# Performance work log

Measured on AMD Instinct MI355X. Metric: run time of the kernel, lower is better.

The kernel has to match this reference:

```python
import jax, jax.numpy as jnp
import numpy as np
import math

H, M, N = 64, 128, 128  # volume dims (m == n required by original index math)
K_NEIGH = 9
W_WIN = 3


def build_neighbor_ids(h, n, w):
    # Periodic (wrap-around) neighbor indices, matching extract_neighbour_indices
    # with m == n. Loop order: z-major, then y, then x, offsets -1..1 for w=3.
    half = w // 2
    offs = list(range(-half, half + 1))
    zi = jnp.arange(h)[:, None, None]
    yi = jnp.arange(n)[None, :, None]
    xi = jnp.arange(n)[None, None, :]
    cols = []
    for oz in offs:
        for oy in offs:
            for ox in offs:
                idx = ((zi + oz) % h) * (n * n) + ((yi + oy) % n) * n + ((xi + ox) % n)
                cols.append(idx.reshape(-1))
    return jnp.stack(cols, axis=1).astype(jnp.int32)  # [P, w^3]


def setup_inputs() -> dict:
    key = jax.random.key(0)
    k1, _ = jax.random.split(key)
    inp = jax.random.normal(k1, (H, M, N), dtype=jnp.float32)
    ksigma = jnp.ones((1, 1, 1, 1), dtype=jnp.float32)  # nn.Parameter init to sigma_m=1.0
    return {"input": inp, "ksigma": ksigma, "k": K_NEIGH, "w": W_WIN}


def reference(input, ksigma, k, w):
    h, m, n = input.shape
    ID = build_neighbor_ids(h, n, w)               # [P, nN]
    anat = input.reshape(-1)                       # [P]
    # get_knn: absolute intensity differences to each neighbor
    dist = jnp.abs(anat[ID] - anat[:, None])       # [P, nN]
    order = jnp.argsort(dist, axis=-1, stable=True)
    sID = jnp.take_along_axis(ID, order, axis=1)   # sorted neighbor indices
    IDk = sID[:, :k]                               # [P, k] top-k nearest by intensity
    Wk = anat[IDk]                                 # [P, k] neighbor intensities (feature rows)
    # get_features: per-row std (torch.std is unbiased, ddof=1)
    sigma = jnp.std(Wk, axis=1, ddof=1)            # [P]
    sigma_safe = jnp.where(sigma == 0, 1.0, sigma)
    neigh = Wk[IDk]                                # [P, k, k] gather feature rows of knn
    diff = Wk[:, None, :] - neigh + 1e-6           # pairwise_distance eps added to diff
    norm = jnp.sqrt(jnp.sum(diff * diff, axis=-1)) # [P, k] L2 pairwise distance
    ks = ksigma.reshape(())
    logits = -jnp.square(norm / sigma_safe[:, None] / (math.sqrt(2.0) * ks))
    logits = jnp.where(sigma[:, None] == 0, 0.0, logits)  # zero row -> uniform softmax
    Kw = jax.nn.softmax(logits, axis=1)            # [P, k] normalized kernel weights
    return Kw
```

## Files before the change

kernel.cpp:

```cpp
#include <hip/hip_runtime.h>
#include <hip/hip_fp16.h>
#include <array>

constexpr int HZ   = 64;
constexpr int NN   = 128;
constexpr int P    = HZ * NN * NN;
constexpr int KSEL = 9;
constexpr int NCOL = 27;
constexpr int STD  = 8;

typedef _Float16 f16x2 __attribute__((ext_vector_type(2)));

constexpr int TY = 10;
constexpr int TX = 34;

constexpr int compute_nce(int n) {
  int t = 0; while ((1 << t) < n) ++t;
  int cnt = 0;
  for (int p = 1 << (t - 1); p > 0; p >>= 1) {
    int q = 1 << (t - 1), r = 0, d = p;
    while (true) {
      for (int i = 0; i < n - d; ++i)
        if ((i & p) == r) ++cnt;
      if (q == p) break;
      d = q - p; r = p; q >>= 1;
    }
  }
  return cnt;
}
constexpr int NCE_FULL = compute_nce(NCOL);

struct CEPair { unsigned char a, b; };
constexpr std::array<CEPair, NCE_FULL> make_net() {
  std::array<CEPair, NCE_FULL> net{};
  int t = 0; while ((1 << t) < NCOL) ++t;
  int k = 0;
  for (int p = 1 << (t - 1); p > 0; p >>= 1) {
    int q = 1 << (t - 1), r = 0, d = p;
    while (true) {
      for (int i = 0; i < NCOL - d; ++i)
        if ((i & p) == r) {
          net[k].a = (unsigned char)i;
          net[k].b = (unsigned char)(i + d);
          ++k;
        }
      if (q == p) break;
      d = q - p; r = p; q >>= 1;
    }
  }
  return net;
}
constexpr auto FULLNET = make_net();

constexpr int count_pruned() {
  bool needed[NCOL] = {};
  for (int i = 0; i < KSEL; ++i) needed[i] = true;
  int cnt = 0;
  for (int e = NCE_FULL - 1; e >= 0; --e) {
    const int a = FULLNET[e].a, b = FULLNET[e].b;
    if (needed[a] || needed[b]) { needed[a] = true; needed[b] = true; ++cnt; }
  }
  return cnt;
}
constexpr int NCE = count_pruned();

constexpr std::array<CEPair, NCE> make_pruned() {
  bool needed[NCOL] = {};
  for (int i = 0; i < KSEL; ++i) needed[i] = true;
  std::array<bool, NCE_FULL> keep{};
  for (int e = NCE_FULL - 1; e >= 0; --e) {
    const int a = FULLNET[e].a, b = FULLNET[e].b;
    if (needed[a] || needed[b]) { keep[e] = true; needed[a] = true; needed[b] = true; }
  }
  std::array<CEPair, NCE> out{};
  int k = 0;
  for (int e = 0; e < NCE_FULL; ++e) if (keep[e]) out[k++] = FULLNET[e];
  return out;
}
constexpr auto NET = make_pruned();

__global__ __launch_bounds__(256) void topk8(
    const float* __restrict__ anat,
    unsigned* __restrict__ rows) {
  __shared__ float in_t[3 * TY * TX];
  __shared__ unsigned lrow[256 * STD];
  const int tid = threadIdx.x;

  const int blk = blockIdx.x;
  const int swz = ((blk & 7) << 9) | (blk >> 3);
  const int z    = swz >> 6;
  const int rest = swz & 63;
  const int y0   = ((rest >> 2) & 15) << 3;
  const int x0   = (rest & 3) << 5;
  const int xl   = tid & 31;
  const int yl   = tid >> 5;

  #pragma unroll
  for (int s = 0; s < 4; ++s) {
    const unsigned q = (unsigned)(s * 256 + tid);
    if (q < (unsigned)(3 * TY * TX)) {
      const unsigned p = q / TX;
      const unsigned r = q - p * TX;
      const unsigned pz = p / TY;
      const int zi = (int)pz, yi = (int)(p - TY * pz);
      const int zz = (z + zi - 1) & (HZ - 1);
      const int yy = (y0 + yi - 1) & (NN - 1);
      const int xg = (x0 - 1 + (int)r) & (NN - 1);
      in_t[q] = anat[(zz << 14) | (yy << 7) | xg];
    }
  }
  __syncthreads();

  const int base = (yl * TX) + xl;
  const float center = in_t[base + 1 * (TY * TX) + 1 * TX + 1];

  unsigned long long key[NCOL];
  #pragma unroll
  for (int c = 0; c < NCOL; ++c) {
    const int czi = c / 9, cyi = (c / 3) % 3, cxi = c % 3;
    const float v = in_t[base + czi * (TY * TX) + cyi * TX + cxi];
    const unsigned vb = __float_as_uint(v);
    const unsigned db = __float_as_uint(v - center) & 0x7fffffffu;
    const unsigned lo32 = ((unsigned)c << 27) | (vb >> 5);
    key[c] = ((unsigned long long)db << 32) | lo32;
  }

  #pragma unroll
  for (int e = 0; e < NCE; ++e) {
    const int a = NET[e].a, b = NET[e].b;
    const double ka = __builtin_bit_cast(double, key[a]);
    const double kb = __builtin_bit_cast(double, key[b]);
    key[a] = __builtin_bit_cast(unsigned long long, fmin(ka, kb));
    key[b] = __builtin_bit_cast(unsigned long long, fmax(ka, kb));
  }

  unsigned d[5] = {0, 0, 0, 0, 0};
  unsigned lo = 0, hi = 0;
  #pragma unroll
  for (int s = 0; s < KSEL; ++s) {
    const unsigned kl = (unsigned)key[s];
    const unsigned c  = (kl >> 27) & 31u;
    const unsigned vb = (kl & 0x07ffffffu) << 5;
    const ushort hb = __half_as_ushort(__float2half(__uint_as_float(vb)));
    d[s >> 1] |= (unsigned)hb << ((s & 1) * 16);
    if (s < 6) lo |= c << (5 * s);
    else       hi |= c << (5 * (s - 6));
  }

  unsigned* myrow = &lrow[tid * STD];
  ((uint4*)myrow)[0] = make_uint4(d[0], d[1], d[2], d[3]);
  ((uint4*)myrow)[1] = make_uint4(d[4], lo, hi, 0u);

  __syncthreads();

  uint4* rows4 = (uint4*)rows;
  const uint4* l4 = (const uint4*)lrow;
  #pragma unroll
  for (int s = 0; s < 2; ++s) {
    const unsigned q   = (unsigned)(s * 256 + tid);
    const unsigned run = q >> 6;
    const unsigned off = q & 63u;
    const unsigned vb  = (unsigned)((z << 14) | ((y0 + (int)run) << 7) | x0);
    rows4[(size_t)vb * 2 + off] = l4[run * 64 + off];
  }
}

constexpr int TROWS = 3 * TY * TX;

__global__ __launch_bounds__(256) void weights8(
    const unsigned* __restrict__ rows,
    const float* __restrict__ ksig,
    float* __restrict__ out) {
  __shared__ unsigned tile[TROWS * STD];
  const int tid = threadIdx.x;

  const int blk = blockIdx.x;
  const int swz = ((blk & 7) << 9) | (blk >> 3);
  const int z    = swz >> 6;
  const int rest = swz & 63;
  const int y0   = ((rest >> 2) & 15) << 3;
  const int x0   = (rest & 3) << 5;
  const int xl   = tid & 31;
  const int yl   = tid >> 5;

  const uint4* rows4 = (const uint4*)rows;
  uint4* t4 = (uint4*)tile;
  #pragma unroll
  for (int s = 0; s < 8; ++s) {
    const unsigned q = (unsigned)(s * 256 + tid);
    if (q < 2040u) {
      const unsigned p   = q / 68u;
      const unsigned rem = q - p * 68u;
      const unsigned r   = rem >> 1;
      const unsigned c   = rem & 1u;
      const unsigned pz  = p / 10u;
      const int zi = (int)pz, yi = (int)(p - 10u * pz);
      const int zz = (z + zi - 1) & (HZ - 1);
      const int yy = (y0 + yi - 1) & (NN - 1);
      const int xg = (x0 - 1 + (int)r) & (NN - 1);
      t4[q] = rows4[(size_t)((zz << 14) | (yy << 7) | xg) * 2 + c];
    }
  }
  __syncthreads();

  const int rho_own = (TY + (yl + 1)) * TX + (xl + 1);
  const uint4 u0 = t4[rho_own * 2], u1 = t4[rho_own * 2 + 1];
  f16x2 wh[5];
  wh[0] = __builtin_bit_cast(f16x2, u0.x);
  wh[1] = __builtin_bit_cast(f16x2, u0.y);
  wh[2] = __builtin_bit_cast(f16x2, u0.z);
  wh[3] = __builtin_bit_cast(f16x2, u0.w);
  wh[4] = __builtin_bit_cast(f16x2, u1.x);
  const unsigned lo = u1.y;
  const unsigned hi = u1.z;

  int rho[KSEL];
  #pragma unroll
  for (int j = 0; j < KSEL; ++j) {
    const unsigned c = (j < 6) ? ((lo >> (5 * j)) & 31u)
                               : ((hi >> (5 * (j - 6))) & 31u);
    const unsigned czi = (c * 57u) >> 9;
    const unsigned rem = c - 9u * czi;
    const unsigned cyi = (rem * 11u) >> 5;
    const unsigned cxi = rem - 3u * cyi;
    rho[j] = (int)czi * (TY * TX) + (yl + (int)cyi) * TX + (xl + (int)cxi);
  }
  uint4 nbuf[KSEL][2];
  #pragma unroll
  for (int j = 0; j < KSEL; ++j) {
    nbuf[j][0] = t4[rho[j] * 2];
    nbuf[j][1] = t4[rho[j] * 2 + 1];
  }

  float ws[KSEL];
  #pragma unroll
  for (int l = 0; l < KSEL; ++l) ws[l] = (float)wh[l >> 1][l & 1];
  float mean = 0.f;
  #pragma unroll
  for (int l = 0; l < KSEL; ++l) mean += ws[l];
  mean *= (1.0f / 9.0f);
  float var = 0.f;
  #pragma unroll
  for (int l = 0; l < KSEL; ++l) { const float t = ws[l] - mean; var += t * t; }
  var *= (1.0f / 8.0f);
  const float sigma = sqrtf(var);

  const float ks = ksig[0];
  const float inv = (sigma == 0.f) ? 0.f : 1.0f / (2.0f * ks * ks * sigma * sigma);

  const _Float16 epsh = (_Float16)1e-6f;
  const f16x2 eps2 = {epsh, epsh};

  float logit[KSEL];
  #pragma unroll
  for (int j = 0; j < KSEL; ++j) {
    const f16x2 nh0 = __builtin_bit_cast(f16x2, nbuf[j][0].x);
    const f16x2 nh1 = __builtin_bit_cast(f16x2, nbuf[j][0].y);
    const f16x2 nh2 = __builtin_bit_cast(f16x2, nbuf[j][0].z);
    const f16x2 nh3 = __builtin_bit_cast(f16x2, nbuf[j][0].w);
    const f16x2 nh4 = __builtin_bit_cast(f16x2, nbuf[j][1].x);
    float s = 0.f;
    f16x2 dd;
    dd = (wh[0] - nh0) + eps2; s = __builtin_amdgcn_fdot2(dd, dd, s, false);
    dd = (wh[1] - nh1) + eps2; s = __builtin_amdgcn_fdot2(dd, dd, s, false);
    dd = (wh[2] - nh2) + eps2; s = __builtin_amdgcn_fdot2(dd, dd, s, false);
    dd = (wh[3] - nh3) + eps2; s = __builtin_amdgcn_fdot2(dd, dd, s, false);
    dd = (wh[4] - nh4) + eps2; s = __builtin_amdgcn_fdot2(dd, dd, s, false);
    logit[j] = -s * inv;
  }

  float mx = logit[0];
  #pragma unroll
  for (int j = 1; j < KSEL; ++j) mx = fmaxf(mx, logit[j]);
  float sum = 0.f;
  float e[KSEL];
  #pragma unroll
  for (int j = 0; j < KSEL; ++j) { e[j] = __expf(logit[j] - mx); sum += e[j]; }
  const float rs = 1.0f / sum;

  __syncthreads();
  float* tf = (float*)tile;
  #pragma unroll
  for (int j = 0; j < KSEL; ++j) tf[tid * KSEL + j] = e[j] * rs;
  __syncthreads();

  const float4* tf4 = (const float4*)tile;
  #pragma unroll
  for (int s = 0; s < 3; ++s) {
    const unsigned q = (unsigned)(s * 256 + tid);
    if (q < 576u) {
      const unsigned row = q / 72u;
      const unsigned f   = q - row * 72u;
      const unsigned vb  = (unsigned)((z << 14) | ((y0 + (int)row) << 7) | x0);
      ((float4*)out)[(size_t)(vb >> 2) * 9 + f] = tf4[row * 72 + f];
    }
  }
}

extern "C" void kernel_launch(void* const* d_in, const int* in_sizes, int n_in,
                              void* d_out, int out_size, void* d_ws, size_t ws_size,
                              hipStream_t stream) {
  const float* anat = (const float*)d_in[0];
  const float* ksig = (const float*)d_in[1];
  unsigned* rows = (unsigned*)d_ws;

  const int blocks = P / 256;
  topk8<<<blocks, 256, 0, stream>>>(anat, rows);
  weights8<<<blocks, 256, 0, stream>>>(rows, ksig, (float*)d_out);
}
```

Before: 122.4 us.

## Split intermediate rows into SoA planes and stage halo via direct global-to-LDS loads

The 32-byte per-voxel intermediate record becomes three planes: 16 bytes of packed fp16 values, a 4-byte word with the ninth value plus the high indices, and a separate 4-byte low-index word that only the owning voxel reads. Neighbour halos in both kernels are staged with global_load_lds direct-to-LDS transfers instead of going through registers, and topk writes its rows directly without an LDS transpose or extra barrier. The aim is to cut workspace traffic from 32 to 24 bytes per voxel, avoid loading unused halo index data, shrink LDS so the weights kernel can fit more blocks per CU (launch bounds hint 5), and lower register pressure. In exchange, the per-thread direct stores are less contiguous than the old LDS-staged copy, and global_load_lds carries its own alignment and ordering rules.

```diff
diff --git a/kernel.cpp b/kernel.cpp
--- a/kernel.cpp
+++ b/kernel.cpp
@@ -7,12 +7,12 @@
 constexpr int P    = HZ * NN * NN;
 constexpr int KSEL = 9;
 constexpr int NCOL = 27;
-constexpr int STD  = 8;
 
 typedef _Float16 f16x2 __attribute__((ext_vector_type(2)));
 
 constexpr int TY = 10;
 constexpr int TX = 34;
+constexpr int TROWS = 3 * TY * TX;
 
 constexpr int compute_nce(int n) {
   int t = 0; while ((1 << t) < n) ++t;
@@ -79,11 +79,22 @@
 }
 constexpr auto NET = make_pruned();
 
-__global__ __launch_bounds__(256) void topk8(
+typedef const __attribute__((address_space(1))) unsigned GU;
+typedef __attribute__((address_space(3))) unsigned LU;
+
+__device__ __forceinline__ void g2l16(const void* g, void* l) {
+  __builtin_amdgcn_global_load_lds((GU*)g, (LU*)l, 16, 0, 0);
+}
+__device__ __forceinline__ void g2l4(const void* g, void* l) {
+  __builtin_amdgcn_global_load_lds((GU*)g, (LU*)l, 4, 0, 0);
+}
+
+__global__ __launch_bounds__(256) void topk9(
     const float* __restrict__ anat,
-    unsigned* __restrict__ rows) {
-  __shared__ float in_t[3 * TY * TX];
-  __shared__ unsigned lrow[256 * STD];
+    uint4* __restrict__ rowsA,
+    unsigned* __restrict__ rowsB0,
+    unsigned* __restrict__ rowsB1) {
+  __shared__ float in_t[TROWS];
   const int tid = threadIdx.x;
 
   const int blk = blockIdx.x;
@@ -98,7 +109,7 @@
   #pragma unroll
   for (int s = 0; s < 4; ++s) {
     const unsigned q = (unsigned)(s * 256 + tid);
-    if (q < (unsigned)(3 * TY * TX)) {
+    if (q < (unsigned)TROWS) {
       const unsigned p = q / TX;
       const unsigned r = q - p * TX;
       const unsigned pz = p / TY;
@@ -106,7 +117,7 @@
       const int zz = (z + zi - 1) & (HZ - 1);
       const int yy = (y0 + yi - 1) & (NN - 1);
       const int xg = (x0 - 1 + (int)r) & (NN - 1);
-      in_t[q] = anat[(zz << 14) | (yy << 7) | xg];
+      g2l4(&anat[(zz << 14) | (yy << 7) | xg], &in_t[q]);
     }
   }
   __syncthreads();
@@ -134,44 +145,35 @@
     key[b] = __builtin_bit_cast(unsigned long long, fmax(ka, kb));
   }
 
-  unsigned d[5] = {0, 0, 0, 0, 0};
-  unsigned lo = 0, hi = 0;
+  unsigned od[4] = {0, 0, 0, 0};
+  unsigned h8 = 0, lo = 0, hi = 0;
   #pragma unroll
   for (int s = 0; s < KSEL; ++s) {
     const unsigned kl = (unsigned)key[s];
     const unsigned c  = (kl >> 27) & 31u;
-    const unsigned vb = (kl & 0x07ffffffu) << 5;
-    const ushort hb = __half_as_ushort(__float2half(__uint_as_float(vb)));
-    d[s >> 1] |= (unsigned)hb << ((s & 1) * 16);
+    const unsigned vbits = (kl & 0x07ffffffu) << 5;
+    const unsigned hb = (unsigned)__half_as_ushort(__float2half(__uint_as_float(vbits)));
+    if (s < 8) od[s >> 1] |= hb << ((s & 1) * 16);
+    else       h8 = hb;
     if (s < 6) lo |= c << (5 * s);
     else       hi |= c << (5 * (s - 6));
   }
 
-  unsigned* myrow = &lrow[tid * STD];
-  ((uint4*)myrow)[0] = make_uint4(d[0], d[1], d[2], d[3]);
-  ((uint4*)myrow)[1] = make_uint4(d[4], lo, hi, 0u);
-
-  __syncthreads();
-
-  uint4* rows4 = (uint4*)rows;
-  const uint4* l4 = (const uint4*)lrow;
-  #pragma unroll
-  for (int s = 0; s < 2; ++s) {
-    const unsigned q   = (unsigned)(s * 256 + tid);
-    const unsigned run = q >> 6;
-    const unsigned off = q & 63u;
-    const unsigned vb  = (unsigned)((z << 14) | ((y0 + (int)run) << 7) | x0);
-    rows4[(size_t)vb * 2 + off] = l4[run * 64 + off];
-  }
-}
-
-constexpr int TROWS = 3 * TY * TX;
-
-__global__ __launch_bounds__(256) void weights8(
-    const unsigned* __restrict__ rows,
+  const unsigned vb = (unsigned)((z << 14) | ((y0 + yl) << 7) | (x0 + xl));
+  rowsA[vb]  = make_uint4(od[0], od[1], od[2], od[3]);
+  rowsB0[vb] = h8 | (hi << 16);
+  rowsB1[vb] = lo;
+}
+
+__global__ __launch_bounds__(256, 5) void weights9(
+    const uint4* __restrict__ rowsA,
+    const unsigned* __restrict__ rowsB0,
+    const unsigned* __restrict__ rowsB1,
     const float* __restrict__ ksig,
     float* __restrict__ out) {
-  __shared__ unsigned tile[TROWS * STD];
+  __shared__ unsigned tile[TROWS * 5];
+  unsigned* tA  = tile;
+  unsigned* tB0 = tile + TROWS * 4;
   const int tid = threadIdx.x;
 
   const int blk = blockIdx.x;
@@ -183,36 +185,37 @@
   const int xl   = tid & 31;
   const int yl   = tid >> 5;
 
-  const uint4* rows4 = (const uint4*)rows;
-  uint4* t4 = (uint4*)tile;
-  #pragma unroll
-  for (int s = 0; s < 8; ++s) {
+  const unsigned vb_own = (unsigned)((z << 14) | ((y0 + yl) << 7) | (x0 + xl));
+  const unsigned lo = rowsB1[vb_own];
+
+  #pragma unroll
+  for (int s = 0; s < 4; ++s) {
     const unsigned q = (unsigned)(s * 256 + tid);
-    if (q < 2040u) {
-      const unsigned p   = q / 68u;
-      const unsigned rem = q - p * 68u;
-      const unsigned r   = rem >> 1;
-      const unsigned c   = rem & 1u;
-      const unsigned pz  = p / 10u;
-      const int zi = (int)pz, yi = (int)(p - 10u * pz);
+    if (q < (unsigned)TROWS) {
+      const unsigned p = q / TX;
+      const unsigned r = q - p * TX;
+      const unsigned pz = p / TY;
+      const int zi = (int)pz, yi = (int)(p - TY * pz);
       const int zz = (z + zi - 1) & (HZ - 1);
       const int yy = (y0 + yi - 1) & (NN - 1);
       const int xg = (x0 - 1 + (int)r) & (NN - 1);
-      t4[q] = rows4[(size_t)((zz << 14) | (yy << 7) | xg) * 2 + c];
+      const unsigned vb = (unsigned)((zz << 14) | (yy << 7) | xg);
+      g2l16(&rowsA[vb],  &tA[q * 4]);
+      g2l4 (&rowsB0[vb], &tB0[q]);
     }
   }
   __syncthreads();
 
   const int rho_own = (TY + (yl + 1)) * TX + (xl + 1);
-  const uint4 u0 = t4[rho_own * 2], u1 = t4[rho_own * 2 + 1];
+  const uint4 a = *(const uint4*)&tA[rho_own * 4];
+  const unsigned b0 = tB0[rho_own];
   f16x2 wh[5];
-  wh[0] = __builtin_bit_cast(f16x2, u0.x);
-  wh[1] = __builtin_bit_cast(f16x2, u0.y);
-  wh[2] = __builtin_bit_cast(f16x2, u0.z);
-  wh[3] = __builtin_bit_cast(f16x2, u0.w);
-  wh[4] = __builtin_bit_cast(f16x2, u1.x);
-  const unsigned lo = u1.y;
-  const unsigned hi = u1.z;
+  wh[0] = __builtin_bit_cast(f16x2, a.x);
+  wh[1] = __builtin_bit_cast(f16x2, a.y);
+  wh[2] = __builtin_bit_cast(f16x2, a.z);
+  wh[3] = __builtin_bit_cast(f16x2, a.w);
+  wh[4] = __builtin_bit_cast(f16x2, b0 & 0xffffu);
+  const unsigned hi = b0 >> 16;
 
   int rho[KSEL];
   #pragma unroll
@@ -225,11 +228,12 @@
     const unsigned cxi = rem - 3u * cyi;
     rho[j] = (int)czi * (TY * TX) + (yl + (int)cyi) * TX + (xl + (int)cxi);
   }
-  uint4 nbuf[KSEL][2];
+  uint4 na[KSEL];
+  unsigned nb[KSEL];
   #pragma unroll
   for (int j = 0; j < KSEL; ++j) {
-    nbuf[j][0] = t4[rho[j] * 2];
-    nbuf[j][1] = t4[rho[j] * 2 + 1];
+    na[j] = *(const uint4*)&tA[rho[j] * 4];
+    nb[j] = tB0[rho[j]];
   }
 
   float ws[KSEL];
@@ -254,11 +258,11 @@
   float logit[KSEL];
   #pragma unroll
   for (int j = 0; j < KSEL; ++j) {
-    const f16x2 nh0 = __builtin_bit_cast(f16x2, nbuf[j][0].x);
-    const f16x2 nh1 = __builtin_bit_cast(f16x2, nbuf[j][0].y);
-    const f16x2 nh2 = __builtin_bit_cast(f16x2, nbuf[j][0].z);
-    const f16x2 nh3 = __builtin_bit_cast(f16x2, nbuf[j][0].w);
-    const f16x2 nh4 = __builtin_bit_cast(f16x2, nbuf[j][1].x);
+    const f16x2 nh0 = __builtin_bit_cast(f16x2, na[j].x);
+    const f16x2 nh1 = __builtin_bit_cast(f16x2, na[j].y);
+    const f16x2 nh2 = __builtin_bit_cast(f16x2, na[j].z);
+    const f16x2 nh3 = __builtin_bit_cast(f16x2, na[j].w);
+    const f16x2 nh4 = __builtin_bit_cast(f16x2, nb[j] & 0xffffu);
     float s = 0.f;
     f16x2 dd;
     dd = (wh[0] - nh0) + eps2; s = __builtin_amdgcn_fdot2(dd, dd, s, false);
@@ -302,9 +306,11 @@
                               hipStream_t stream) {
   const float* anat = (const float*)d_in[0];
   const float* ksig = (const float*)d_in[1];
-  unsigned* rows = (unsigned*)d_ws;
+  uint4* rowsA      = (uint4*)d_ws;
+  unsigned* rowsB0  = (unsigned*)d_ws + (size_t)4 * P;
+  unsigned* rowsB1  = rowsB0 + P;
 
   const int blocks = P / 256;
-  topk8<<<blocks, 256, 0, stream>>>(anat, rows);
-  weights8<<<blocks, 256, 0, stream>>>(rows, ksig, (float*)d_out);
-}
+  topk9<<<blocks, 256, 0, stream>>>(anat, rowsA, rowsB0, rowsB1);
+  weights9<<<blocks, 256, 0, stream>>>(rowsA, rowsB0, rowsB1, ksig, (float*)d_out);
+}
```

Measured after the change: 108.4 us. -11.5%, faster.
